# Optimization experiments

Measured on AMD Instinct MI355X. Metric: run time of the kernel, lower is better.

## Reference

```python
import jax, jax.numpy as jnp
import numpy as np

K = 3
STRIDE = 1
PADDING = 1
INVALID = -1.0


def _unfold(x, k, stride, padding, fill):
    # x: [B, C, H, W] -> patches [B, C, k, k, P] matching torch F.unfold ordering
    x = jnp.pad(x, ((0, 0), (0, 0), (padding, padding), (padding, padding)),
                constant_values=fill)
    # feature dim ordered channel-major (C, kh, kw), same as torch unfold
    p = jax.lax.conv_general_dilated_patches(x, (k, k), (stride, stride), 'VALID')
    b, _, ho, wo = p.shape
    c = x.shape[1]
    return p.reshape(b, c, k, k, ho * wo), ho, wo


def setup_inputs() -> dict:
    key = jax.random.key(0)
    k1, k2, k3, k4 = jax.random.split(key, 4)
    B, C, H, W = 8, 64, 128, 128
    OC = 64
    inp = jax.random.normal(k1, (B, C, H, W), dtype=jnp.float32)
    mask = jax.random.randint(k2, (B, H, W), 0, 4).astype(jnp.float32)
    conv = jax.random.normal(k3, (OC, C, K, K), dtype=jnp.float32) * 0.05
    bias = jax.random.normal(k4, (OC,), dtype=jnp.float32) * 0.05
    return {"inp": inp, "mask": mask, "conv": conv, "bias": bias}


def reference(inp, mask, conv, bias):
    k, stride, padding = K, STRIDE, PADDING
    b, c, h_in, w_in = inp.shape
    oc = conv.shape[0]
    center = (k - 1) // 2

    inp_patched, ho, wo = _unfold(inp, k, stride, padding, INVALID)       # [B,C,k,k,P]
    mask_patched, _, _ = _unfold(mask[:, None], k, stride, padding, INVALID)  # [B,1,k,k,P]
    mask_patched = mask_patched[:, 0]                                      # [B,k,k,P]

    center_val = mask_patched[:, center:center + 1, center:center + 1, :]  # [B,1,1,P]
    mask_eq = (mask_patched == center_val).astype(inp.dtype)               # [B,k,k,P]

    masked_input = inp_patched * mask_eq[:, None]                          # [B,C,k,k,P]
    m_norm = (k * k) / jnp.clip(mask_eq.reshape(b, k * k, -1).sum(axis=1), 1e-8)  # [B,P]

    masked_input = masked_input.reshape(b, c, k * k, -1)                   # [B,C,kk,P]
    w = conv.reshape(oc, c, k * k)                                         # [O,C,kk]
    out = jnp.einsum('bcxp,ocx->bop', masked_input, w)                     # [B,O,P]
    out = out * m_norm[:, None, :]
    out = out.reshape(b, oc, ho, wo)
    out = out + bias[None, :, None, None]

    mask_out = mask_patched[:, center, center, :].reshape(b, 1, ho, wo)
    return out, mask_out
```

## Files before the change

kernel.cpp:

```cpp
#include <hip/hip_runtime.h>
#include <stdint.h>

#define HW   128
#define CIN  64
#define OCN  64
#define NB   8

typedef __attribute__((ext_vector_type(8)))  short short8;
typedef __attribute__((ext_vector_type(16))) float floatx16;

union F8 { short8 s; uint32_t d[4]; uint4 q; };

static __device__ __forceinline__ ushort f2bf(float f) {
    uint32_t u = __float_as_uint(f);
    return (ushort)((u + 0x7FFFu + ((u >> 16) & 1u)) >> 16);
}

#define LROW_STR 68

__global__ __launch_bounds__(256)
void prep_kernel(const float* __restrict__ inp, const float* __restrict__ conv,
                 ushort* __restrict__ wb, ushort* __restrict__ xb)
{
    __shared__ ushort Ls[HW * LROW_STR];
    const int bid = blockIdx.x, tid = threadIdx.x;

    if (bid >= 1024) {
        int t = bid - 1024;
        #pragma unroll
        for (int i = 0; i < 16; ++i) {
            int id = i * 256 + tid;
            int oc = id >> 6, c = id & 63;
            wb[t * 4096 + id] = f2bf(conv[(oc * 64 + c) * 9 + t]);
        }
        return;
    }

    const int bb = bid >> 7, y = bid & 127;
    const int cg = tid >> 5, xg = tid & 31;
    const float* src = inp + ((size_t)(bb * CIN + cg * 8) * HW + y) * HW + xg * 4;
    #pragma unroll
    for (int k = 0; k < 8; ++k) {
        float4 v = *(const float4*)(src + (size_t)k * HW * HW);
        ushort* p = Ls + (xg * 4) * LROW_STR + cg * 8 + k;
        p[0]            = f2bf(v.x);
        p[LROW_STR]     = f2bf(v.y);
        p[2 * LROW_STR] = f2bf(v.z);
        p[3 * LROW_STR] = f2bf(v.w);
    }
    __syncthreads();
    ushort* dst = xb + (size_t)(bb * HW + y) * HW * 64;
    const int g = tid & 7, p0 = tid >> 3;
    #pragma unroll
    for (int pass = 0; pass < 4; ++pass) {
        int p = pass * 32 + p0;
        uint2 a = *(const uint2*)(Ls + p * LROW_STR + g * 8);
        uint2 b = *(const uint2*)(Ls + p * LROW_STR + g * 8 + 4);
        *(uint4*)(dst + p * 64 + g * 8) = make_uint4(a.x, a.y, b.x, b.y);
    }
}

static __device__ __forceinline__ void load_tap(
    const ushort* __restrict__ wb, const ushort* __restrict__ xb,
    int t, int bb, int y, int x0, int x1, int l31, int lh,
    uint4* Ar, uint4* Br)
{
    const ushort* wp = wb + t * 4096 + l31 * 64 + lh * 8;
    #pragma unroll
    for (int h = 0; h < 2; ++h)
        #pragma unroll
        for (int ks = 0; ks < 4; ++ks)
            Ar[h * 4 + ks] = *(const uint4*)(wp + h * 2048 + ks * 16);

    const int dy = t / 3 - 1, dx = t % 3 - 1;
    int ny = y + dy; ny = ny < 0 ? 0 : (ny > HW - 1 ? HW - 1 : ny);
    #pragma unroll
    for (int n = 0; n < 2; ++n) {
        int nx = (n ? x1 : x0) + dx;
        nx = nx < 0 ? 0 : (nx > HW - 1 ? HW - 1 : nx);
        const ushort* bp = xb + (((size_t)bb * HW + ny) * HW + nx) * 64 + lh * 8;
        #pragma unroll
        for (int ks = 0; ks < 4; ++ks)
            Br[n * 4 + ks] = *(const uint4*)(bp + ks * 16);
    }
}

__global__ __launch_bounds__(64, 2)
void iconv_main(const ushort* __restrict__ xb, const ushort* __restrict__ wb,
                const float* __restrict__ mask, const float* __restrict__ bias,
                float* __restrict__ out)
{
    const int bid = blockIdx.x;
    const int bb = bid >> 8, y = (bid >> 1) & 127, xw = (bid & 1) * 64;
    const int lane = threadIdx.x, l31 = lane & 31, lh = lane >> 5;
    const int x0 = xw + l31, x1 = x0 + 32;

    const float* mrow = mask + ((size_t)bb * HW + y) * HW;
    const float m00 = mrow[x0], m01 = mrow[x1];
    uint32_t bits0 = 0, bits1 = 0;
    #pragma unroll
    for (int t = 0; t < 9; ++t) {
        int dy = t / 3 - 1, dx = t % 3 - 1;
        int ny = y + dy;
        bool vy = (ny >= 0) && (ny < HW);
        int nyc = vy ? ny : y;
        const float* r = mask + ((size_t)bb * HW + nyc) * HW;
        int nx0 = x0 + dx, nx1 = x1 + dx;
        bool ok0 = vy && (nx0 >= 0) && (nx0 < HW);
        bool ok1 = vy && (nx1 >= 0) && (nx1 < HW);
        int c0 = nx0 < 0 ? 0 : (nx0 > HW - 1 ? HW - 1 : nx0);
        int c1 = nx1 < 0 ? 0 : (nx1 > HW - 1 ? HW - 1 : nx1);
        if (ok0 && r[c0] == m00) bits0 |= 1u << t;
        if (ok1 && r[c1] == m01) bits1 |= 1u << t;
    }
    const float norm0 = 9.0f / (float)__popc(bits0);
    const float norm1 = 9.0f / (float)__popc(bits1);

    float* mout = out + (size_t)NB * OCN * HW * HW + ((size_t)bb * HW + y) * HW;
    mout[x0] = m00;
    mout[x1] = m01;

    floatx16 acc00 = {0,0,0,0,0,0,0,0,0,0,0,0,0,0,0,0};
    floatx16 acc01 = {0,0,0,0,0,0,0,0,0,0,0,0,0,0,0,0};
    floatx16 acc10 = {0,0,0,0,0,0,0,0,0,0,0,0,0,0,0,0};
    floatx16 acc11 = {0,0,0,0,0,0,0,0,0,0,0,0,0,0,0,0};

    uint4 Ar[2][8], Br[2][8];
    load_tap(wb, xb, 0, bb, y, x0, x1, l31, lh, Ar[0], Br[0]);

    #pragma unroll
    for (int t = 0; t < 9; ++t) {
        const int buf = t & 1;
        if (t < 8)
            load_tap(wb, xb, t + 1, bb, y, x0, x1, l31, lh, Ar[buf ^ 1], Br[buf ^ 1]);

        const uint32_t s0 = ((bits0 >> t) & 1u) ? 0xFFFFFFFFu : 0u;
        const uint32_t s1 = ((bits1 >> t) & 1u) ? 0xFFFFFFFFu : 0u;

        #pragma unroll
        for (int ks = 0; ks < 4; ++ks) {
            F8 a0, a1, b0, b1;
            a0.q = Ar[buf][ks];
            a1.q = Ar[buf][4 + ks];
            b0.q = Br[buf][ks];
            b1.q = Br[buf][4 + ks];
            b0.d[0] &= s0; b0.d[1] &= s0; b0.d[2] &= s0; b0.d[3] &= s0;
            b1.d[0] &= s1; b1.d[1] &= s1; b1.d[2] &= s1; b1.d[3] &= s1;
            acc00 = __builtin_amdgcn_mfma_f32_32x32x16_bf16(a0.s, b0.s, acc00, 0, 0, 0);
            acc01 = __builtin_amdgcn_mfma_f32_32x32x16_bf16(a0.s, b1.s, acc01, 0, 0, 0);
            acc10 = __builtin_amdgcn_mfma_f32_32x32x16_bf16(a1.s, b0.s, acc10, 0, 0, 0);
            acc11 = __builtin_amdgcn_mfma_f32_32x32x16_bf16(a1.s, b1.s, acc11, 0, 0, 0);
        }
    }

    float* outp = out + (size_t)bb * OCN * HW * HW + (size_t)y * HW;
    #pragma unroll
    for (int mt = 0; mt < 2; ++mt) {
        #pragma unroll
        for (int nt = 0; nt < 2; ++nt) {
            floatx16 a = (mt == 0) ? (nt == 0 ? acc00 : acc01)
                                   : (nt == 0 ? acc10 : acc11);
            float nm = (nt == 0) ? norm0 : norm1;
            int x = xw + nt * 32 + l31;
            #pragma unroll
            for (int r = 0; r < 16; ++r) {
                int oc = mt * 32 + (r & 3) + 8 * (r >> 2) + 4 * lh;
                outp[(size_t)oc * (HW * HW) + x] = a[r] * nm + bias[oc];
            }
        }
    }
}

extern "C" void kernel_launch(void* const* d_in, const int* in_sizes, int n_in,
                              void* d_out, int out_size, void* d_ws, size_t ws_size,
                              hipStream_t stream) {
    (void)in_sizes; (void)n_in; (void)out_size; (void)ws_size;
    const float* inp  = (const float*)d_in[0];
    const float* mask = (const float*)d_in[1];
    const float* conv = (const float*)d_in[2];
    const float* bias = (const float*)d_in[3];
    float* out = (float*)d_out;

    ushort* wb = (ushort*)d_ws;
    ushort* xb = (ushort*)d_ws + 65536;

    prep_kernel<<<1033, 256, 0, stream>>>(inp, conv, wb, xb);
    iconv_main<<<NB * HW * 2, 64, 0, stream>>>(xb, wb, mask, bias, out);
}
```

Baseline: 129.0 us.

## Stage input rows in LDS via global_load_lds and swizzle channel layout

The main conv kernel now runs 4-wave blocks that each cover two output rows. The blocks stage the four needed input rows (bf16, 64 KB) into LDS with global_load_lds, and all nine taps read B operands from LDS instead of from global memory. The prep kernel drops its LDS transpose and writes the channel-contiguous layout directly from registers, using an XOR swizzle on 8-channel slots to avoid LDS bank conflicts. This trades redundant global loads across taps for LDS reuse, but uses 64 KB LDS per block, which may limit occupancy.

```diff
diff --git a/kernel.cpp b/kernel.cpp
--- a/kernel.cpp
+++ b/kernel.cpp
@@ -16,15 +16,11 @@
     return (ushort)((u + 0x7FFFu + ((u >> 16) & 1u)) >> 16);
 }
 
-#define LROW_STR 68
-
 __global__ __launch_bounds__(256)
 void prep_kernel(const float* __restrict__ inp, const float* __restrict__ conv,
                  ushort* __restrict__ wb, ushort* __restrict__ xb)
 {
-    __shared__ ushort Ls[HW * LROW_STR];
     const int bid = blockIdx.x, tid = threadIdx.x;
-
     if (bid >= 1024) {
         int t = bid - 1024;
         #pragma unroll
@@ -35,65 +31,60 @@
         }
         return;
     }
-
     const int bb = bid >> 7, y = bid & 127;
-    const int cg = tid >> 5, xg = tid & 31;
+    const int cg = tid & 7;
+    const int xg = tid >> 3;
     const float* src = inp + ((size_t)(bb * CIN + cg * 8) * HW + y) * HW + xg * 4;
-    #pragma unroll
-    for (int k = 0; k < 8; ++k) {
-        float4 v = *(const float4*)(src + (size_t)k * HW * HW);
-        ushort* p = Ls + (xg * 4) * LROW_STR + cg * 8 + k;
-        p[0]            = f2bf(v.x);
-        p[LROW_STR]     = f2bf(v.y);
-        p[2 * LROW_STR] = f2bf(v.z);
-        p[3 * LROW_STR] = f2bf(v.w);
-    }
-    __syncthreads();
+    float4 v[8];
+    #pragma unroll
+    for (int k = 0; k < 8; ++k)
+        v[k] = *(const float4*)(src + (size_t)k * HW * HW);
+    const float* fv = (const float*)v;
     ushort* dst = xb + (size_t)(bb * HW + y) * HW * 64;
-    const int g = tid & 7, p0 = tid >> 3;
-    #pragma unroll
-    for (int pass = 0; pass < 4; ++pass) {
-        int p = pass * 32 + p0;
-        uint2 a = *(const uint2*)(Ls + p * LROW_STR + g * 8);
-        uint2 b = *(const uint2*)(Ls + p * LROW_STR + g * 8 + 4);
-        *(uint4*)(dst + p * 64 + g * 8) = make_uint4(a.x, a.y, b.x, b.y);
-    }
-}
-
-static __device__ __forceinline__ void load_tap(
-    const ushort* __restrict__ wb, const ushort* __restrict__ xb,
-    int t, int bb, int y, int x0, int x1, int l31, int lh,
-    uint4* Ar, uint4* Br)
-{
-    const ushort* wp = wb + t * 4096 + l31 * 64 + lh * 8;
-    #pragma unroll
-    for (int h = 0; h < 2; ++h)
-        #pragma unroll
-        for (int ks = 0; ks < 4; ++ks)
-            Ar[h * 4 + ks] = *(const uint4*)(wp + h * 2048 + ks * 16);
-
-    const int dy = t / 3 - 1, dx = t % 3 - 1;
-    int ny = y + dy; ny = ny < 0 ? 0 : (ny > HW - 1 ? HW - 1 : ny);
-    #pragma unroll
-    for (int n = 0; n < 2; ++n) {
-        int nx = (n ? x1 : x0) + dx;
-        nx = nx < 0 ? 0 : (nx > HW - 1 ? HW - 1 : nx);
-        const ushort* bp = xb + (((size_t)bb * HW + ny) * HW + nx) * 64 + lh * 8;
-        #pragma unroll
-        for (int ks = 0; ks < 4; ++ks)
-            Br[n * 4 + ks] = *(const uint4*)(bp + ks * 16);
-    }
-}
-
-__global__ __launch_bounds__(64, 2)
+    #pragma unroll
+    for (int j = 0; j < 4; ++j) {
+        int px = xg * 4 + j;
+        uint32_t d0 = (uint32_t)f2bf(fv[0 * 4 + j]) | ((uint32_t)f2bf(fv[1 * 4 + j]) << 16);
+        uint32_t d1 = (uint32_t)f2bf(fv[2 * 4 + j]) | ((uint32_t)f2bf(fv[3 * 4 + j]) << 16);
+        uint32_t d2 = (uint32_t)f2bf(fv[4 * 4 + j]) | ((uint32_t)f2bf(fv[5 * 4 + j]) << 16);
+        uint32_t d3 = (uint32_t)f2bf(fv[6 * 4 + j]) | ((uint32_t)f2bf(fv[7 * 4 + j]) << 16);
+        int slot = cg ^ (px & 7);
+        *(uint4*)(dst + px * 64 + slot * 8) = make_uint4(d0, d1, d2, d3);
+    }
+}
+
+#define LDS_BYTES 65536
+
+__global__ __launch_bounds__(256, 2)
 void iconv_main(const ushort* __restrict__ xb, const ushort* __restrict__ wb,
                 const float* __restrict__ mask, const float* __restrict__ bias,
                 float* __restrict__ out)
 {
-    const int bid = blockIdx.x;
-    const int bb = bid >> 8, y = (bid >> 1) & 127, xw = (bid & 1) * 64;
-    const int lane = threadIdx.x, l31 = lane & 31, lh = lane >> 5;
-    const int x0 = xw + l31, x1 = x0 + 32;
+    extern __shared__ char smem[];
+    ushort* Ls = (ushort*)smem;
+
+    const int tid  = threadIdx.x;
+    const int bb   = blockIdx.x >> 6;
+    const int y0   = (blockIdx.x & 63) << 1;
+    const int lane = tid & 63, l31 = lane & 31, lh = lane >> 5;
+    const int w    = tid >> 6;
+    const int yloc = w >> 1, xh = w & 1;
+    const int y    = y0 + yloc, xw = xh * 64;
+    const int x0   = xw + l31, x1 = x0 + 32;
+
+    {
+        int gy = y0 - 1 + w;
+        gy = gy < 0 ? 0 : (gy > HW - 1 ? HW - 1 : gy);
+        const ushort* grow = xb + ((size_t)(bb * HW + gy) * HW) * 64;
+        ushort* lrow = Ls + w * 8192;
+        #pragma unroll
+        for (int i = 0; i < 16; ++i) {
+            __builtin_amdgcn_global_load_lds(
+                (const __attribute__((address_space(1))) uint32_t*)(grow + i * 512 + lane * 8),
+                (__attribute__((address_space(3))) uint32_t*)(lrow + i * 512),
+                16, 0, 0);
+        }
+    }
 
     const float* mrow = mask + ((size_t)bb * HW + y) * HW;
     const float m00 = mrow[x0], m01 = mrow[x1];
@@ -120,20 +111,39 @@
     mout[x0] = m00;
     mout[x1] = m01;
 
+    uint4 Ar[2][8];
+    #pragma unroll
+    for (int i = 0; i < 8; ++i) {
+        int h = i >> 2, ks = i & 3;
+        Ar[0][i] = *(const uint4*)(wb + (l31 + h * 32) * 64 + ks * 16 + lh * 8);
+    }
+
+    __syncthreads();
+
     floatx16 acc00 = {0,0,0,0,0,0,0,0,0,0,0,0,0,0,0,0};
     floatx16 acc01 = {0,0,0,0,0,0,0,0,0,0,0,0,0,0,0,0};
     floatx16 acc10 = {0,0,0,0,0,0,0,0,0,0,0,0,0,0,0,0};
     floatx16 acc11 = {0,0,0,0,0,0,0,0,0,0,0,0,0,0,0,0};
 
-    uint4 Ar[2][8], Br[2][8];
-    load_tap(wb, xb, 0, bb, y, x0, x1, l31, lh, Ar[0], Br[0]);
-
     #pragma unroll
     for (int t = 0; t < 9; ++t) {
         const int buf = t & 1;
-        if (t < 8)
-            load_tap(wb, xb, t + 1, bb, y, x0, x1, l31, lh, Ar[buf ^ 1], Br[buf ^ 1]);
-
+        if (t < 8) {
+            const ushort* wp = wb + (t + 1) * 4096;
+            #pragma unroll
+            for (int i = 0; i < 8; ++i) {
+                int h = i >> 2, ks = i & 3;
+                Ar[buf ^ 1][i] = *(const uint4*)(wp + (l31 + h * 32) * 64 + ks * 16 + lh * 8);
+            }
+        }
+
+        const int dy = t / 3 - 1, dx = t % 3 - 1;
+        const int rrB = 1 + yloc + dy;
+        int p0 = x0 + dx; p0 = p0 < 0 ? 0 : (p0 > HW - 1 ? HW - 1 : p0);
+        int p1 = x1 + dx; p1 = p1 < 0 ? 0 : (p1 > HW - 1 ? HW - 1 : p1);
+        const ushort* b0b = Ls + rrB * 8192 + p0 * 64;
+        const ushort* b1b = Ls + rrB * 8192 + p1 * 64;
+        const int sw0 = p0 & 7, sw1 = p1 & 7;
         const uint32_t s0 = ((bits0 >> t) & 1u) ? 0xFFFFFFFFu : 0u;
         const uint32_t s1 = ((bits1 >> t) & 1u) ? 0xFFFFFFFFu : 0u;
 
@@ -142,8 +152,8 @@
             F8 a0, a1, b0, b1;
             a0.q = Ar[buf][ks];
             a1.q = Ar[buf][4 + ks];
-            b0.q = Br[buf][ks];
-            b1.q = Br[buf][4 + ks];
+            b0.q = *(const uint4*)(b0b + (((2 * ks + lh) ^ sw0) * 8));
+            b1.q = *(const uint4*)(b1b + (((2 * ks + lh) ^ sw1) * 8));
             b0.d[0] &= s0; b0.d[1] &= s0; b0.d[2] &= s0; b0.d[3] &= s0;
             b1.d[0] &= s1; b1.d[1] &= s1; b1.d[2] &= s1; b1.d[3] &= s1;
             acc00 = __builtin_amdgcn_mfma_f32_32x32x16_bf16(a0.s, b0.s, acc00, 0, 0, 0);
@@ -184,6 +194,9 @@
     ushort* wb = (ushort*)d_ws;
     ushort* xb = (ushort*)d_ws + 65536;
 
+    hipFuncSetAttribute((const void*)iconv_main,
+                        hipFuncAttributeMaxDynamicSharedMemorySize, LDS_BYTES);
+
     prep_kernel<<<1033, 256, 0, stream>>>(inp, conv, wb, xb);
-    iconv_main<<<NB * HW * 2, 64, 0, stream>>>(xb, wb, mask, bias, out);
-}
+    iconv_main<<<NB * (HW / 2), 256, LDS_BYTES, stream>>>(xb, wb, mask, bias, out);
+}
```

Measured after the change: 117.3 us. 9.1% less time.
